# Optimization experiments

Hardware: AMD Instinct MI355X
Metric: run time of the kernel (lower is better)

## Reference

```python
import jax, jax.numpy as jnp
import numpy as np

T, B, NHID = 64, 32, 768
NB, BS = 6, 128          # num_blocks, block_size = nhid // num_blocks
TOPK = 4                 # active blocks per step
NTOK = 32000
ATT = 4 * BS             # input-attention value dim (att_out), per RIMs BlocksCore
DK = 64                  # input-attention key dim
NH2, DK2 = 4, 16         # communication attention heads / head dim


def setup_inputs() -> dict:
    key = jax.random.key(0)
    ks = jax.random.split(key, 16)
    s = 0.02
    return {
        "x": jax.random.normal(ks[0], (T, B, NHID), jnp.float32),
        "hx0": jax.random.normal(ks[1], (B, NHID), jnp.float32),
        "cx0": jax.random.normal(ks[2], (B, NHID), jnp.float32),
        # input attention (1 head): per-read-block query proj, per-write-slot key/value proj
        "Wq_in": jax.random.normal(ks[3], (NB, BS, DK), jnp.float32) * s,
        "Wk_in": jax.random.normal(ks[4], (2, NHID, DK), jnp.float32) * s,
        "Wv_in": jax.random.normal(ks[5], (2, NHID, ATT), jnp.float32) * s,
        # block-diagonal LSTM (blockify_params): per-block weights
        "Wih": jax.random.normal(ks[6], (NB, ATT, 4 * BS), jnp.float32) * s,
        "Whh": jax.random.normal(ks[7], (NB, BS, 4 * BS), jnp.float32) * s,
        "b_lstm": jnp.zeros((NB, 4 * BS), jnp.float32),
        # communication attention (4 heads, dk=dv=16), per-block projections + output proj
        "Wq_c": jax.random.normal(ks[8], (NB, BS, NH2 * DK2), jnp.float32) * s,
        "Wk_c": jax.random.normal(ks[9], (NB, BS, NH2 * DK2), jnp.float32) * s,
        "Wv_c": jax.random.normal(ks[10], (NB, BS, NH2 * DK2), jnp.float32) * s,
        "Wo_c": jax.random.normal(ks[11], (NB, NH2 * DK2, BS), jnp.float32) * s,
        # decoder
        "Wd": jax.random.normal(ks[12], (NTOK, NHID), jnp.float32) * 0.1,
        "bd": jnp.zeros((NTOK,), jnp.float32),
    }


def _step(hx, cx, xt, Wq_in, Wk_in, Wv_in, Wih, Whh, b_lstm, Wq_c, Wk_c, Wv_c, Wo_c):
    hb = hx.reshape(B, NB, BS)
    cb = cx.reshape(B, NB, BS)
    # --- input attention: each block reads from {null, input} slots ---
    kv_in = jnp.stack([jnp.zeros_like(xt), xt], axis=1)          # [B,2,NHID]
    q = jnp.einsum('bnd,ndk->bnk', hb, Wq_in)                    # [B,NB,DK]
    k = jnp.einsum('bmd,mdk->bmk', kv_in, Wk_in)                 # [B,2,DK]
    v = jnp.einsum('bmd,mdv->bmv', kv_in, Wv_in)                 # [B,2,ATT]
    iatt = jax.nn.softmax(
        jnp.einsum('bnk,bmk->bnm', q, k) / jnp.sqrt(jnp.float32(DK)), axis=-1)
    inp_use = jnp.einsum('bnm,bmv->bnv', iatt, v)                # [B,NB,ATT]
    # --- top-k block routing: drop NB-TOPK blocks attending most to null ---
    null_att = iatt[:, :, 0]                                     # [B,NB]
    _, drop_idx = jax.lax.top_k(null_att, NB - TOPK)
    mask = jnp.ones((B, NB), hx.dtype).at[
        jnp.arange(B)[:, None], drop_idx].set(0.0)               # [B,NB]
    # --- per-block (block-diagonal) LSTM ---
    gates = (jnp.einsum('bnv,nvg->bng', inp_use, Wih)
             + jnp.einsum('bnh,nhg->bng', hb, Whh) + b_lstm)     # [B,NB,4*BS]
    i, f, g, o = jnp.split(gates, 4, axis=-1)
    c_new = jax.nn.sigmoid(f) * cb + jax.nn.sigmoid(i) * jnp.tanh(g)
    h_new = jax.nn.sigmoid(o) * jnp.tanh(c_new)                  # [B,NB,BS]
    # --- communication attention among blocks (residual) ---
    q2 = jnp.einsum('bnd,ndk->bnk', h_new, Wq_c).reshape(B, NB, NH2, DK2)
    k2 = jnp.einsum('bnd,ndk->bnk', h_new, Wk_c).reshape(B, NB, NH2, DK2)
    v2 = jnp.einsum('bnd,ndk->bnk', h_new, Wv_c).reshape(B, NB, NH2, DK2)
    att = jax.nn.softmax(
        jnp.einsum('bihk,bjhk->bhij', q2, k2) / jnp.sqrt(jnp.float32(DK2)), axis=-1)
    comm = jnp.einsum('bhij,bjhv->bihv', att, v2).reshape(B, NB, NH2 * DK2)
    h_new = h_new + jnp.einsum('bnk,nkd->bnd', comm, Wo_c)
    # --- gated state update: inactive blocks keep old state ---
    m = mask[:, :, None]
    hx_next = (m * h_new + (1.0 - m) * hb).reshape(B, NHID)
    cx_next = (m * c_new + (1.0 - m) * cb).reshape(B, NHID)
    return hx_next, cx_next


def reference(x, hx0, cx0, Wq_in, Wk_in, Wv_in, Wih, Whh, b_lstm,
              Wq_c, Wk_c, Wv_c, Wo_c, Wd, bd):
    def scan_step(carry, xt):
        hx, cx = carry
        hx, cx = _step(hx, cx, xt, Wq_in, Wk_in, Wv_in, Wih, Whh, b_lstm,
                       Wq_c, Wk_c, Wv_c, Wo_c)
        return (hx, cx), hx
    (hx, cx), outs = jax.lax.scan(scan_step, (hx0, cx0), x)     # outs: [T,B,NHID]
    decoded = outs.reshape(T * B, NHID) @ Wd.T + bd              # [T*B,NTOK]
    return decoded, hx, cx
```

## Files before the change

kernel.cpp:

```cpp
#include <hip/hip_runtime.h>
#include <hip/hip_bf16.h>
#include <stdint.h>

#define TT 64
#define BB 32
#define NHIDC 768
#define NBK 6
#define BSZ 128
#define NTOKC 32000

using f32x4  = __attribute__((ext_vector_type(4))) float;
using f32x2  = __attribute__((ext_vector_type(2))) float;
using short8 = __attribute__((ext_vector_type(8))) short;

#define OFF_FLG   0u
#define OFF_XPUB  4096u
#define OFF_HTB   8065024u
#define OFF_K1    11210752u
#define OFF_V1    11735040u
#define OFF_U     15929344u
#define OFF_WDB   41095168u

__device__ __forceinline__ float sigf(float x){ return 1.f/(1.f + expf(-x)); }

__device__ __forceinline__ void stc(float* p, float v){
  __hip_atomic_store(p, v, __ATOMIC_RELAXED, __HIP_MEMORY_SCOPE_AGENT);
}
__device__ __forceinline__ float ldc(const float* p){
  return __hip_atomic_load(p, __ATOMIC_RELAXED, __HIP_MEMORY_SCOPE_AGENT);
}
#define VMCNT0 asm volatile("s_waitcnt vmcnt(0)" ::: "memory")
#define CBAR   asm volatile("" ::: "memory")

__device__ __forceinline__ void gload16(const void* g, void* l){
  __builtin_amdgcn_global_load_lds(
      (const __attribute__((address_space(1))) unsigned int*)g,
      (__attribute__((address_space(3))) unsigned int*)l, 16, 0, 0);
}

__device__ __forceinline__ int xslot(int par, int gg, int nn, int b){
  return (((par*16 + gg)*6 + nn)*2 + b)*132;
}

__global__ void prep_kernel(const float* __restrict__ Wd,
                            unsigned short* __restrict__ Wdb,
                            unsigned int* __restrict__ flags)
{
  if (blockIdx.x == 0 && threadIdx.x < 128)
    __hip_atomic_store(flags + threadIdx.x, 0u, __ATOMIC_RELAXED, __HIP_MEMORY_SCOPE_AGENT);
  int i = blockIdx.x*blockDim.x + threadIdx.x;
  const int n4 = NTOKC*NHIDC/4;
  const int stride = gridDim.x*blockDim.x;
  for (; i < n4; i += stride){
    const float4 v = ((const float4*)Wd)[i];
    ushort4 o;
    __hip_bfloat16 b0 = __float2bfloat16(v.x); o.x = *reinterpret_cast<unsigned short*>(&b0);
    __hip_bfloat16 b1 = __float2bfloat16(v.y); o.y = *reinterpret_cast<unsigned short*>(&b1);
    __hip_bfloat16 b2 = __float2bfloat16(v.z); o.z = *reinterpret_cast<unsigned short*>(&b2);
    __hip_bfloat16 b3 = __float2bfloat16(v.w); o.w = *reinterpret_cast<unsigned short*>(&b3);
    ((ushort4*)Wdb)[i] = o;
  }
}

template<int TM, int TN>
__global__ __launch_bounds__(256) void gemm_f32(
    const float* __restrict__ A, int lda,
    const float* __restrict__ B, int ldb, long bstride,
    float* __restrict__ C, int ldc, long cstride,
    int N, int K)
{
  constexpr int BM = 16*TM, BN = 16*TN;
  __shared__ float As[16][BM];
  __shared__ float Bs[16][BN+4];
  const float* Bb = B + (long)blockIdx.z * bstride;
  float* Cb = C + (long)blockIdx.z * cstride;
  const int m0 = blockIdx.x*BM, n0 = blockIdx.y*BN;
  const int tid = threadIdx.x, tx = tid & 15, ty = tid >> 4;
  float acc[TM][TN];
  #pragma unroll
  for (int i=0;i<TM;++i)
    #pragma unroll
    for (int j=0;j<TN;++j) acc[i][j]=0.f;

  for (int k0=0; k0<K; k0+=16){
    if constexpr (TM == 8){
      const int r = tid>>1, kk = (tid&1)*8;
      const float4 v0 = *(const float4*)&A[(long)(m0+r)*lda + k0 + kk];
      const float4 v1 = *(const float4*)&A[(long)(m0+r)*lda + k0 + kk + 4];
      As[kk+0][r]=v0.x; As[kk+1][r]=v0.y; As[kk+2][r]=v0.z; As[kk+3][r]=v0.w;
      As[kk+4][r]=v1.x; As[kk+5][r]=v1.y; As[kk+6][r]=v1.z; As[kk+7][r]=v1.w;
    } else {
      const int r = tid>>2, kk = (tid&3)*4;
      const float4 v0 = *(const float4*)&A[(long)(m0+r)*lda + k0 + kk];
      As[kk+0][r]=v0.x; As[kk+1][r]=v0.y; As[kk+2][r]=v0.z; As[kk+3][r]=v0.w;
    }
    if constexpr (TN == 8){
      const int rb = tid>>4, cb = (tid&15)*8;
      float4 v0 = {0,0,0,0}, v1 = {0,0,0,0};
      if (n0+cb+4 <= N) v0 = *(const float4*)&Bb[(long)(k0+rb)*ldb + n0+cb];
      if (n0+cb+8 <= N) v1 = *(const float4*)&Bb[(long)(k0+rb)*ldb + n0+cb+4];
      *(float4*)&Bs[rb][cb]   = v0;
      *(float4*)&Bs[rb][cb+4] = v1;
    } else {
      const int rb = tid>>4, cb = (tid&15)*4;
      float4 v0 = {0,0,0,0};
      if (n0+cb+4 <= N) v0 = *(const float4*)&Bb[(long)(k0+rb)*ldb + n0+cb];
      *(float4*)&Bs[rb][cb] = v0;
    }
    __syncthreads();
    #pragma unroll
    for (int kk=0; kk<16; ++kk){
      float av[TM], bv[TN];
      #pragma unroll
      for (int i=0;i<TM;++i) av[i] = As[kk][ty*TM+i];
      #pragma unroll
      for (int j=0;j<TN;++j) bv[j] = Bs[kk][tx*TN+j];
      #pragma unroll
      for (int i=0;i<TM;++i)
        #pragma unroll
        for (int j=0;j<TN;++j) acc[i][j] += av[i]*bv[j];
    }
    __syncthreads();
  }
  #pragma unroll
  for (int i=0;i<TM;++i){
    const int row = m0 + ty*TM + i;
    #pragma unroll
    for (int j=0;j<TN;++j){
      const int col = n0 + tx*TN + j;
      if (col < N) Cb[(long)row*ldc + col] = acc[i][j];
    }
  }
}

__global__ __launch_bounds__(1024, 2) void recurrent_kernel(
    const float* __restrict__ hx0, const float* __restrict__ cx0,
    const float* __restrict__ Wq_in, const float* __restrict__ Whh,
    const float* __restrict__ b_lstm,
    const float* __restrict__ Wk_c, const float* __restrict__ Wv_c,
    const float* __restrict__ Wq_c, const float* __restrict__ Wo_c,
    const float* __restrict__ K1buf, const float* __restrict__ Ubuf,
    float* __restrict__ xpub, unsigned int* __restrict__ flags,
    unsigned short* __restrict__ HTx,
    float* __restrict__ out_hx, float* __restrict__ out_cx)
{
  const int w = blockIdx.x, gg = w/6, n = w - gg*6, tid = threadIdx.x;

  __shared__ float WcT[192*130];
  __shared__ float WqL[128*65];
  __shared__ float hL[2][128], cL[2][128], h0L[2][128], cnL[2][128];
  __shared__ float partL[2][2][512];
  __shared__ float uL[2][512];
  __shared__ float blL[512];
  __shared__ float kvqL[2][192];
  __shared__ float kvAll[2][6][130];
  __shared__ float commL[2][64];
  __shared__ float nullAll[2][8];
  __shared__ float sL[2], maskL[2];

  const int kh = tid >> 9, gc = tid & 511;
  const int od = tid >> 3, okq = tid & 7;

  f32x4 whr[16];
  {
    const float* src = Whh + (long)n*65536 + kh*64*512 + gc;
    #pragma unroll
    for (int r4=0; r4<16; ++r4){
      f32x4 v;
      v[0] = src[(r4*4+0)*512]; v[1] = src[(r4*4+1)*512];
      v[2] = src[(r4*4+2)*512]; v[3] = src[(r4*4+3)*512];
      whr[r4] = v;
    }
  }
  #pragma unroll
  for (int i=0;i<16;++i) asm volatile("" : "+v"(whr[i]));
  f32x4 wo0, wo1;
  {
    const float* src = Wo_c + n*8192 + od;
    #pragma unroll
    for (int j=0;j<4;++j) wo0[j] = src[(okq*8+j)*128];
    #pragma unroll
    for (int j=0;j<4;++j) wo1[j] = src[(okq*8+4+j)*128];
  }
  asm volatile("" : "+v"(wo0));
  asm volatile("" : "+v"(wo1));

  if (tid < 512) blL[tid] = b_lstm[n*512 + tid];
  for (int i = tid; i < 8192; i += 1024){
    const int h = i>>6, c = i&63;
    WcT[(c    )*130 + h] = Wk_c[n*8192 + i];
    WcT[(c+ 64)*130 + h] = Wv_c[n*8192 + i];
    WcT[(c+128)*130 + h] = Wq_c[n*8192 + i];
    WqL[h*65 + c] = Wq_in[n*8192 + i];
  }
  if (tid < 256){
    const int b = tid>>7, d = tid&127;
    hL[b][d] = hx0[(gg*2+b)*768 + n*128 + d];
    cL[b][d] = cx0[(gg*2+b)*768 + n*128 + d];
  }
  __syncthreads();

  for (int t = 0; t < TT; ++t){
    const int par = t & 1;
    uL[kh][gc] = Ubuf[((long)(t*32 + gg*2 + kh)*6 + n)*512 + gc];
    float k1r = 0.f;
    if (tid < 128) k1r = K1buf[(long)(t*32 + gg*2 + (tid>>6))*64 + (tid&63)];

    {
      float gd0 = 0.f, gd1 = 0.f;
      #pragma unroll
      for (int r4 = 0; r4 < 16; ++r4){
        const f32x4 h0v = *(const f32x4*)&hL[0][kh*64 + r4*4];
        const f32x4 h1v = *(const f32x4*)&hL[1][kh*64 + r4*4];
        #pragma unroll
        for (int j=0;j<4;++j){
          gd0 += whr[r4][j]*h0v[j];
          gd1 += whr[r4][j]*h1v[j];
        }
      }
      partL[0][kh][gc] = gd0;
      partL[1][kh][gc] = gd1;
    }
    if (tid < 128){
      const int b = tid>>6, k = tid&63;
      float q = 0.f;
      #pragma unroll 16
      for (int h=0; h<128; ++h) q += WqL[h*65 + k]*hL[b][h];
      float term = q*k1r;
      #pragma unroll
      for (int off=32; off; off>>=1) term += __shfl_xor(term, off);
      if (k == 0){
        const float l1 = term*0.125f;
        const float mx = fmaxf(l1, 0.f);
        const float e0 = expf(0.f-mx), e1 = expf(l1-mx);
        const float inv = 1.f/(e0+e1);
        sL[b] = e1*inv;
        stc(&xpub[xslot(par,gg,n,b) + 128], e0*inv);
      }
    }
    __syncthreads();
    if (tid < 256){
      const int b = tid>>7, dd = tid&127;
      const float s = sL[b];
      const float gi = partL[b][0][dd]     + partL[b][1][dd]     + s*uL[b][dd]     + blL[dd];
      const float gf = partL[b][0][128+dd] + partL[b][1][128+dd] + s*uL[b][128+dd] + blL[128+dd];
      const float gG = partL[b][0][256+dd] + partL[b][1][256+dd] + s*uL[b][256+dd] + blL[256+dd];
      const float go = partL[b][0][384+dd] + partL[b][1][384+dd] + s*uL[b][384+dd] + blL[384+dd];
      const float cp = cL[b][dd];
      const float cn = sigf(gf)*cp + sigf(gi)*tanhf(gG);
      const float h0 = sigf(go)*tanhf(cn);
      cnL[b][dd] = cn; h0L[b][dd] = h0;
    }
    __syncthreads();
    if (tid < 384){
      const int b = tid/192, c = tid%192;
      float a = 0.f;
      #pragma unroll
      for (int h4=0; h4<32; ++h4){
        const f32x2 wa = *(const f32x2*)&WcT[c*130 + h4*4];
        const f32x2 wb = *(const f32x2*)&WcT[c*130 + h4*4 + 2];
        const f32x4 hv = *(const f32x4*)&h0L[b][h4*4];
        a += wa[0]*hv[0] + wa[1]*hv[1] + wb[0]*hv[2] + wb[1]*hv[3];
      }
      kvqL[b][c] = a;
      if (c < 128) stc(&xpub[xslot(par,gg,n,b) + c], a);
    }
    VMCNT0;
    __syncthreads();
    if (tid < 6){
      if (tid == 0)
        __hip_atomic_store(&flags[gg*8+n], (unsigned)(t+1), __ATOMIC_RELAXED, __HIP_MEMORY_SCOPE_AGENT);
      while (__hip_atomic_load(&flags[gg*8+tid], __ATOMIC_RELAXED, __HIP_MEMORY_SCOPE_AGENT) < (unsigned)(t+1))
        __builtin_amdgcn_s_sleep(1);
    }
    __syncthreads(); CBAR;
    for (int idx = tid; idx < 1536; idx += 1024){
      const int j = idx/256, r = idx&255, b = r>>7, c = r&127;
      kvAll[b][j][c] = ldc(&xpub[xslot(par,gg,j,b) + c]);
    }
    if (tid < 12){
      const int j = tid>>1, b = tid&1;
      nullAll[b][j] = ldc(&xpub[xslot(par,gg,j,b) + 128]);
    }
    __syncthreads();
    if (tid < 64){
      const int lane = tid;
      const int g5 = lane>>3, l3 = lane&7;
      const int b = g5>>2, h = g5&3;
      float lg = -1e30f;
      if (l3 < 6){
        float s = 0.f;
        #pragma unroll
        for (int kk=0; kk<16; ++kk)
          s += kvqL[b][128 + h*16 + kk]*kvAll[b][l3][h*16 + kk];
        lg = s*0.25f;
      }
      float mx = lg;
      mx = fmaxf(mx, __shfl_xor(mx,1));
      mx = fmaxf(mx, __shfl_xor(mx,2));
      mx = fmaxf(mx, __shfl_xor(mx,4));
      float ev = (l3 < 6) ? expf(lg - mx) : 0.f;
      float sum = ev;
      sum += __shfl_xor(sum,1); sum += __shfl_xor(sum,2); sum += __shfl_xor(sum,4);
      const float myw = ev/sum;
      float s0 = 0.f, s1 = 0.f;
      #pragma unroll
      for (int j=0;j<6;++j){
        const float wj = __shfl(myw, g5*8 + j);
        s0 += wj*kvAll[b][j][64 + h*16 + l3*2];
        s1 += wj*kvAll[b][j][64 + h*16 + l3*2 + 1];
      }
      commL[b][h*16 + l3*2]     = s0;
      commL[b][h*16 + l3*2 + 1] = s1;
      if (lane < 2){
        const float own = nullAll[lane][n];
        int rank = 0;
        #pragma unroll
        for (int j=0;j<6;++j){
          const float v = nullAll[lane][j];
          rank += (v > own || (v == own && j < n)) ? 1 : 0;
        }
        maskL[lane] = (rank < 2) ? 0.f : 1.f;
      }
    }
    __syncthreads();
    {
      #pragma unroll
      for (int b=0; b<2; ++b){
        float a = 0.f;
        #pragma unroll
        for (int j=0;j<4;++j) a += commL[b][okq*8+j]*wo0[j];
        #pragma unroll
        for (int j=0;j<4;++j) a += commL[b][okq*8+4+j]*wo1[j];
        a += __shfl_xor(a,1); a += __shfl_xor(a,2); a += __shfl_xor(a,4);
        if (okq == 0 && maskL[b] != 0.f){
          hL[b][od] = h0L[b][od] + a;
          cL[b][od] = cnL[b][od];
        }
      }
    }
    __syncthreads();
    if (tid < 256){
      const int b = tid>>7, d = tid&127;
      const float hv = hL[b][d];
      __hip_bfloat16 hb16 = __float2bfloat16(hv);
      HTx[(long)(t*32 + gg*2 + b)*768 + n*128 + d] = *reinterpret_cast<unsigned short*>(&hb16);
      if (t == TT-1){
        out_hx[(gg*2+b)*768 + n*128 + d] = hv;
        out_cx[(gg*2+b)*768 + n*128 + d] = cL[b][d];
      }
    }
  }
}

__global__ __launch_bounds__(256) void decoder_kernel(
    const unsigned short* __restrict__ A,
    const unsigned short* __restrict__ Bw,
    const float* __restrict__ bd,
    float* __restrict__ out)
{
  __shared__ unsigned short As[4096];
  __shared__ unsigned short Bs[4096];
  const int bid = blockIdx.x;
  const int tile = (bid & 7)*500 + (bid >> 3);
  const int m0 = (tile & 15)*128, n0 = (tile >> 4)*128;
  const int tid = threadIdx.x;
  const int wv = tid >> 6, lane = tid & 63;
  const int wm = wv >> 1, wn = wv & 1;
  const int r16 = lane & 15, krow = lane >> 4;

  f32x4 acc[4][4] = {};

  for (int k0 = 0; k0 < 768; k0 += 32){
    #pragma unroll
    for (int i=0; i<2; ++i){
      const int idx = i*256 + tid;
      const int row = idx >> 2, k8 = (idx & 3)*8;
      gload16(&A [(long)(m0+row)*768 + k0 + k8], (char*)As + i*4096 + wv*1024);
      gload16(&Bw[(long)(n0+row)*768 + k0 + k8], (char*)Bs + i*4096 + wv*1024);
    }
    __syncthreads();
    short8 af[4], bf[4];
    #pragma unroll
    for (int mi=0; mi<4; ++mi)
      af[mi] = *(const short8*)&As[(wm*64 + mi*16 + r16)*32 + krow*8];
    #pragma unroll
    for (int ni=0; ni<4; ++ni)
      bf[ni] = *(const short8*)&Bs[(wn*64 + ni*16 + r16)*32 + krow*8];
    #pragma unroll
    for (int mi=0; mi<4; ++mi)
      #pragma unroll
      for (int ni=0; ni<4; ++ni)
        acc[mi][ni] = __builtin_amdgcn_mfma_f32_16x16x32_bf16(af[mi], bf[ni], acc[mi][ni], 0, 0, 0);
    __syncthreads();
  }

  #pragma unroll
  for (int ni=0; ni<4; ++ni){
    const int col = n0 + wn*64 + ni*16 + r16;
    const float bv = bd[col];
    #pragma unroll
    for (int mi=0; mi<4; ++mi){
      const int rbase = m0 + wm*64 + mi*16 + krow*4;
      #pragma unroll
      for (int j=0; j<4; ++j)
        out[(size_t)(rbase + j)*NTOKC + col] = acc[mi][ni][j] + bv;
    }
  }
}

extern "C" void kernel_launch(void* const* d_in, const int* in_sizes, int n_in,
                              void* d_out, int out_size, void* d_ws, size_t ws_size,
                              hipStream_t stream)
{
  (void)in_sizes; (void)n_in; (void)out_size; (void)ws_size;
  const float* x      = (const float*)d_in[0];
  const float* hx0    = (const float*)d_in[1];
  const float* cx0    = (const float*)d_in[2];
  const float* Wq_in  = (const float*)d_in[3];
  const float* Wk_in  = (const float*)d_in[4];
  const float* Wv_in  = (const float*)d_in[5];
  const float* Wih    = (const float*)d_in[6];
  const float* Whh    = (const float*)d_in[7];
  const float* b_lstm = (const float*)d_in[8];
  const float* Wq_c   = (const float*)d_in[9];
  const float* Wk_c   = (const float*)d_in[10];
  const float* Wv_c   = (const float*)d_in[11];
  const float* Wo_c   = (const float*)d_in[12];
  const float* Wd     = (const float*)d_in[13];
  const float* bd     = (const float*)d_in[14];

  char* ws = (char*)d_ws;
  unsigned int*  flg  = (unsigned int*)(ws + OFF_FLG);
  float*         xpub = (float*)(ws + OFF_XPUB);
  unsigned short* HTx = (unsigned short*)(ws + OFF_HTB);
  float*         K1b  = (float*)(ws + OFF_K1);
  float*         V1b  = (float*)(ws + OFF_V1);
  float*         Ub   = (float*)(ws + OFF_U);
  unsigned short* Wdb = (unsigned short*)(ws + OFF_WDB);

  float* out_dec = (float*)d_out;
  float* out_hx  = out_dec + (size_t)2048*NTOKC;
  float* out_cx  = out_hx + BB*NHIDC;

  prep_kernel<<<2048, 256, 0, stream>>>(Wd, Wdb, flg);
  gemm_f32<4,4><<<dim3(32,1,1), 256, 0, stream>>>(x, NHIDC, Wk_in + 768*64, 64, 0,
                                                  K1b, 64, 0, 64, NHIDC);
  gemm_f32<4,4><<<dim3(32,8,1), 256, 0, stream>>>(x, NHIDC, Wv_in + 768*512, 512, 0,
                                                  V1b, 512, 0, 512, NHIDC);
  gemm_f32<8,8><<<dim3(16,4,6), 256, 0, stream>>>(V1b, 512, Wih, 512, (long)512*512,
                                                  Ub, 3072, 512, 512, 512);
  recurrent_kernel<<<96, 1024, 0, stream>>>(hx0, cx0, Wq_in, Whh, b_lstm,
                                            Wk_c, Wv_c, Wq_c, Wo_c,
                                            K1b, Ub, xpub, flg, HTx,
                                            out_hx, out_cx);
  decoder_kernel<<<4000, 256, 0, stream>>>(HTx, Wdb, bd, out_dec);
}
```

Before: 1.311 ms.

## Replace per-step flag barrier with tagged 64-bit data publication

Each published value is now stored as a 64-bit word that packs the float with a step tag. Readers spin on each word until its tag matches the current step, so the separate flag store, the vmcnt drain and the block-wide flag polling stage are removed. A block's own values are read from shared memory instead of global. In exchange, every read is a 64-bit atomic that may poll on its own, the publication buffer doubles in size, and the prep kernel must zero it.

After: 1.273 ms. 1.03x faster.

```diff
diff --git a/kernel.cpp b/kernel.cpp
--- a/kernel.cpp
+++ b/kernel.cpp
@@ -12,8 +12,8 @@
 using f32x4  = __attribute__((ext_vector_type(4))) float;
 using f32x2  = __attribute__((ext_vector_type(2))) float;
 using short8 = __attribute__((ext_vector_type(8))) short;
-
-#define OFF_FLG   0u
+typedef unsigned long long u64;
+
 #define OFF_XPUB  4096u
 #define OFF_HTB   8065024u
 #define OFF_K1    11210752u
@@ -23,14 +23,21 @@
 
 __device__ __forceinline__ float sigf(float x){ return 1.f/(1.f + expf(-x)); }
 
-__device__ __forceinline__ void stc(float* p, float v){
-  __hip_atomic_store(p, v, __ATOMIC_RELAXED, __HIP_MEMORY_SCOPE_AGENT);
-}
-__device__ __forceinline__ float ldc(const float* p){
-  return __hip_atomic_load(p, __ATOMIC_RELAXED, __HIP_MEMORY_SCOPE_AGENT);
-}
-#define VMCNT0 asm volatile("s_waitcnt vmcnt(0)" ::: "memory")
-#define CBAR   asm volatile("" ::: "memory")
+__device__ __forceinline__ void stp(u64* p, float v, unsigned tag){
+  union { float f; unsigned u; } cv; cv.f = v;
+  const u64 pk = ((u64)tag << 32) | cv.u;
+  __hip_atomic_store(p, pk, __ATOMIC_RELAXED, __HIP_MEMORY_SCOPE_AGENT);
+}
+__device__ __forceinline__ float ldp(const u64* p, unsigned tag){
+  u64 v = __hip_atomic_load(p, __ATOMIC_RELAXED, __HIP_MEMORY_SCOPE_AGENT);
+  while ((unsigned)(v >> 32) < tag){
+    __builtin_amdgcn_s_sleep(1);
+    v = __hip_atomic_load(p, __ATOMIC_RELAXED, __HIP_MEMORY_SCOPE_AGENT);
+  }
+  union { unsigned u; float f; } cv; cv.u = (unsigned)v;
+  return cv.f;
+}
+#define CBAR asm volatile("" ::: "memory")
 
 __device__ __forceinline__ void gload16(const void* g, void* l){
   __builtin_amdgcn_global_load_lds(
@@ -44,10 +51,15 @@
 
 __global__ void prep_kernel(const float* __restrict__ Wd,
                             unsigned short* __restrict__ Wdb,
-                            unsigned int* __restrict__ flags)
+                            u64* __restrict__ xpub)
 {
-  if (blockIdx.x == 0 && threadIdx.x < 128)
-    __hip_atomic_store(flags + threadIdx.x, 0u, __ATOMIC_RELAXED, __HIP_MEMORY_SCOPE_AGENT);
+  {
+    int i = blockIdx.x*blockDim.x + threadIdx.x;
+    const int nx = 2*16*6*2*132;
+    const int stride = gridDim.x*blockDim.x;
+    for (; i < nx; i += stride)
+      __hip_atomic_store(xpub + i, 0ull, __ATOMIC_RELAXED, __HIP_MEMORY_SCOPE_AGENT);
+  }
   int i = blockIdx.x*blockDim.x + threadIdx.x;
   const int n4 = NTOKC*NHIDC/4;
   const int stride = gridDim.x*blockDim.x;
@@ -140,7 +152,7 @@
     const float* __restrict__ Wk_c, const float* __restrict__ Wv_c,
     const float* __restrict__ Wq_c, const float* __restrict__ Wo_c,
     const float* __restrict__ K1buf, const float* __restrict__ Ubuf,
-    float* __restrict__ xpub, unsigned int* __restrict__ flags,
+    u64* __restrict__ xpub,
     unsigned short* __restrict__ HTx,
     float* __restrict__ out_hx, float* __restrict__ out_cx)
 {
@@ -156,7 +168,7 @@
   __shared__ float kvAll[2][6][130];
   __shared__ float commL[2][64];
   __shared__ float nullAll[2][8];
-  __shared__ float sL[2], maskL[2];
+  __shared__ float sL[2], nullLoc[2], maskL[2];
 
   const int kh = tid >> 9, gc = tid & 511;
   const int od = tid >> 3, okq = tid & 7;
@@ -202,6 +214,7 @@
 
   for (int t = 0; t < TT; ++t){
     const int par = t & 1;
+    const unsigned tag = (unsigned)(t+1);
     uL[kh][gc] = Ubuf[((long)(t*32 + gg*2 + kh)*6 + n)*512 + gc];
     float k1r = 0.f;
     if (tid < 128) k1r = K1buf[(long)(t*32 + gg*2 + (tid>>6))*64 + (tid&63)];
@@ -235,7 +248,8 @@
         const float e0 = expf(0.f-mx), e1 = expf(l1-mx);
         const float inv = 1.f/(e0+e1);
         sL[b] = e1*inv;
-        stc(&xpub[xslot(par,gg,n,b) + 128], e0*inv);
+        nullLoc[b] = e0*inv;
+        stp(xpub + xslot(par,gg,n,b) + 128, e0*inv, tag);
       }
     }
     __syncthreads();
@@ -263,26 +277,20 @@
         a += wa[0]*hv[0] + wa[1]*hv[1] + wb[0]*hv[2] + wb[1]*hv[3];
       }
       kvqL[b][c] = a;
-      if (c < 128) stc(&xpub[xslot(par,gg,n,b) + c], a);
-    }
-    VMCNT0;
-    __syncthreads();
-    if (tid < 6){
-      if (tid == 0)
-        __hip_atomic_store(&flags[gg*8+n], (unsigned)(t+1), __ATOMIC_RELAXED, __HIP_MEMORY_SCOPE_AGENT);
-      while (__hip_atomic_load(&flags[gg*8+tid], __ATOMIC_RELAXED, __HIP_MEMORY_SCOPE_AGENT) < (unsigned)(t+1))
-        __builtin_amdgcn_s_sleep(1);
-    }
-    __syncthreads(); CBAR;
+      if (c < 128) stp(xpub + xslot(par,gg,n,b) + c, a, tag);
+    }
+    __syncthreads();
     for (int idx = tid; idx < 1536; idx += 1024){
       const int j = idx/256, r = idx&255, b = r>>7, c = r&127;
-      kvAll[b][j][c] = ldc(&xpub[xslot(par,gg,j,b) + c]);
+      if (j == n) kvAll[b][j][c] = kvqL[b][c];
+      else        kvAll[b][j][c] = ldp(xpub + xslot(par,gg,j,b) + c, tag);
     }
     if (tid < 12){
       const int j = tid>>1, b = tid&1;
-      nullAll[b][j] = ldc(&xpub[xslot(par,gg,j,b) + 128]);
-    }
-    __syncthreads();
+      if (j == n) nullAll[b][j] = nullLoc[b];
+      else        nullAll[b][j] = ldp(xpub + xslot(par,gg,j,b) + 128, tag);
+    }
+    __syncthreads(); CBAR;
     if (tid < 64){
       const int lane = tid;
       const int g5 = lane>>3, l3 = lane&7;
@@ -431,8 +439,7 @@
   const float* bd     = (const float*)d_in[14];
 
   char* ws = (char*)d_ws;
-  unsigned int*  flg  = (unsigned int*)(ws + OFF_FLG);
-  float*         xpub = (float*)(ws + OFF_XPUB);
+  u64*           xpub = (u64*)(ws + OFF_XPUB);
   unsigned short* HTx = (unsigned short*)(ws + OFF_HTB);
   float*         K1b  = (float*)(ws + OFF_K1);
   float*         V1b  = (float*)(ws + OFF_V1);
@@ -443,7 +450,7 @@
   float* out_hx  = out_dec + (size_t)2048*NTOKC;
   float* out_cx  = out_hx + BB*NHIDC;
 
-  prep_kernel<<<2048, 256, 0, stream>>>(Wd, Wdb, flg);
+  prep_kernel<<<2048, 256, 0, stream>>>(Wd, Wdb, xpub);
   gemm_f32<4,4><<<dim3(32,1,1), 256, 0, stream>>>(x, NHIDC, Wk_in + 768*64, 64, 0,
                                                   K1b, 64, 0, 64, NHIDC);
   gemm_f32<4,4><<<dim3(32,8,1), 256, 0, stream>>>(x, NHIDC, Wv_in + 768*512, 512, 0,
@@ -452,7 +459,7 @@
                                                   Ub, 3072, 512, 512, 512);
   recurrent_kernel<<<96, 1024, 0, stream>>>(hx0, cx0, Wq_in, Whh, b_lstm,
                                             Wk_c, Wv_c, Wq_c, Wo_c,
-                                            K1b, Ub, xpub, flg, HTx,
+                                            K1b, Ub, xpub, HTx,
                                             out_hx, out_cx);
   decoder_kernel<<<4000, 256, 0, stream>>>(HTx, Wdb, bd, out_dec);
 }
```
